# Performance work log

Hardware: AMD Instinct MI355X
Metric: run time of the kernel (lower is better)

Reference implementation:

```python
import jax, jax.numpy as jnp
import numpy as np

EPS = 1e-5

def layer_norm(x, gamma, beta):
    mu = jnp.mean(x, axis=-1, keepdims=True)
    var = jnp.mean(jnp.square(x - mu), axis=-1, keepdims=True)
    return (x - mu) * jax.lax.rsqrt(var + EPS) * gamma + beta

def reverse_sigmoid(x):
    # torch version clamps value to [0.001, 0.999] with a detached offset ->
    # straight-through: clipped value, identity gradient into the logit.
    y = x + jax.lax.stop_gradient(jnp.clip(x, 0.001, 0.999) - x)
    return jnp.log(y) - jnp.log1p(-y)

def setup_inputs() -> dict:
    key = jax.random.key(0)
    ks = jax.random.split(key, 8)
    N, D, A, F8, FD = 32768, 1024, 256, 8, 64
    inp = {
        "unary_term": jax.random.normal(ks[0], (N, D), jnp.float32),
        "pair_term": jax.random.normal(ks[1], (N, D), jnp.float32),
        "auxiliary_term": jax.random.normal(ks[2], (N, A), jnp.float32),
        "auxiliary_gating_weight": jax.random.uniform(ks[3], (N,), jnp.float32),
        # self.w params: LayerNorm(2D) + Linear(2D, FD)
        "ln_gamma": jnp.ones((2 * D,), jnp.float32),
        "ln_beta": jnp.zeros((2 * D,), jnp.float32),
        "W": jax.random.normal(ks[4], (2 * D, FD), jnp.float32) * 0.02,
        "b": jnp.zeros((FD,), jnp.float32),
        # self.w_aux params: LayerNorm(A) + Linear(A, 8)
        "ln_aux_gamma": jnp.ones((A,), jnp.float32),
        "ln_aux_beta": jnp.zeros((A,), jnp.float32),
        "W_aux": jax.random.normal(ks[5], (A, F8), jnp.float32) * 0.02,
        "b_aux": jnp.zeros((F8,), jnp.float32),
        # use_auxiliary_gate_weight=True -> both init to 0.33
        "gate_weight": jnp.array(0.33, jnp.float32),
        "aux_gate_weight": jnp.array(0.33, jnp.float32),
    }
    return inp

def reference(unary_term, pair_term, auxiliary_term, auxiliary_gating_weight,
              ln_gamma, ln_beta, W, b, ln_aux_gamma, ln_aux_beta, W_aux, b_aux,
              gate_weight, aux_gate_weight):
    # paired_feats = relu(cat([unary, pair], 1))
    paired = jax.nn.relu(jnp.concatenate([unary_term, pair_term], axis=1))  # [N, 2D]
    # gate = sigmoid(Linear(relu(LN(paired))))
    gate = jax.nn.sigmoid(jax.nn.relu(layer_norm(paired, ln_gamma, ln_beta)) @ W + b)  # [N, FD]
    aux_gate = jax.nn.sigmoid(jax.nn.relu(layer_norm(auxiliary_term, ln_aux_gamma, ln_aux_beta)) @ W_aux + b_aux)  # [N, 8]
    gate = jnp.mean(gate, axis=1)        # [N]
    aux_gate = jnp.mean(aux_gate, axis=1)  # [N]
    logit = gate_weight * reverse_sigmoid(gate) + aux_gate_weight * reverse_sigmoid(aux_gate)
    g = jax.nn.sigmoid(logit) * auxiliary_gating_weight  # use_auxiliary_gate_weight=True
    output = pair_term * g[:, None]
    return (output, g)
```

## Files before the change

kernel.cpp:

```cpp
#include <hip/hip_runtime.h>
#include <math.h>


#define EPS_LN 1e-5f

typedef __attribute__((ext_vector_type(8))) short short8;
typedef __attribute__((ext_vector_type(4))) float f32x4;

__device__ __forceinline__ unsigned short f2bf(float f) {
  unsigned int u = __float_as_uint(f);
  u += 0x7FFFu + ((u >> 16) & 1u);
  return (unsigned short)(u >> 16);
}

__device__ __forceinline__ float wsum64(float v) {
  v += __shfl_xor(v, 32);
  v += __shfl_xor(v, 16);
  v += __shfl_xor(v, 8);
  v += __shfl_xor(v, 4);
  v += __shfl_xor(v, 2);
  v += __shfl_xor(v, 1);
  return v;
}

__device__ __forceinline__ float sigmoidf_(float x) {
  return 1.0f / (1.0f + __expf(-x));
}

__device__ __forceinline__ float rsigf(float x) {
  float y = fminf(fmaxf(x, 0.001f), 0.999f);
  return logf(y) - log1pf(-y);
}

__device__ __forceinline__ short nrm1(float x, float g, float b,
                                      float rs, float nmr) {
  float t = fmaxf(x, 0.f);
  float n = fmaf(t, rs, nmr);
  float z = fmaxf(fmaf(n, g, b), 0.f);
  return (short)f2bf(z);
}

__global__ void prep_wfrag(const float* __restrict__ W,
                           unsigned short* __restrict__ wfrag) {
  const int lane = threadIdx.x;
  const int b = blockIdx.x;
  const int ntile = b >> 6;
  const int kb = b & 63;
  const int f = (ntile << 4) + (lane & 15);
  const int kbase = (kb << 5) + ((lane >> 4) << 3);
  unsigned short tmp[8];
#pragma unroll
  for (int j = 0; j < 8; ++j) tmp[j] = f2bf(W[(size_t)(kbase + j) * 64 + f]);
  ushort4* dst = reinterpret_cast<ushort4*>(wfrag + (((size_t)b * 64 + lane) << 3));
  dst[0] = make_ushort4(tmp[0], tmp[1], tmp[2], tmp[3]);
  dst[1] = make_ushort4(tmp[4], tmp[5], tmp[6], tmp[7]);
}

__global__ void __launch_bounds__(256, 4) fused_main(
    const float* __restrict__ unary, const float* __restrict__ pair,
    const float* __restrict__ aux, const float* __restrict__ auxw,
    const float* __restrict__ ln_g, const float* __restrict__ ln_b,
    const float* __restrict__ b_lin,
    const float* __restrict__ ln_ag, const float* __restrict__ ln_ab,
    const float* __restrict__ W_aux, const float* __restrict__ b_aux,
    const float* __restrict__ gw, const float* __restrict__ agw,
    const unsigned short* __restrict__ wfrag,
    float* __restrict__ out, float* __restrict__ out_g) {
  __shared__ float part[4][16][68];
  __shared__ float stat_mu[16];
  __shared__ float stat_rs[16];

  const int tid = threadIdx.x;
  const int w = tid >> 6;
  const int lane = tid & 63;
  const int base = blockIdx.x << 4;

  float auxg0 = 0.f, auxg1 = 0.f, auxg2 = 0.f, auxg3 = 0.f;

  const float4 agv4 = reinterpret_cast<const float4*>(ln_ag)[lane];
  const float4 abv4 = reinterpret_cast<const float4*>(ln_ab)[lane];
  const float bauxl = b_aux[lane & 7];

#pragma unroll
  for (int i = 0; i < 4; ++i) {
    const int rl = (w << 2) + i;
    const int row = base + rl;

    const float4* u4 = reinterpret_cast<const float4*>(unary + (size_t)row * 1024);
    const float4* p4 = reinterpret_cast<const float4*>(pair + (size_t)row * 1024);
    float s = 0.f, sq = 0.f;
#pragma unroll
    for (int j = 0; j < 4; ++j) {
      float4 uv = u4[lane + 64 * j];
      float4 pv = p4[lane + 64 * j];
      uv.x = fmaxf(uv.x, 0.f); uv.y = fmaxf(uv.y, 0.f);
      uv.z = fmaxf(uv.z, 0.f); uv.w = fmaxf(uv.w, 0.f);
      pv.x = fmaxf(pv.x, 0.f); pv.y = fmaxf(pv.y, 0.f);
      pv.z = fmaxf(pv.z, 0.f); pv.w = fmaxf(pv.w, 0.f);
      s += uv.x + uv.y + uv.z + uv.w;
      s += pv.x + pv.y + pv.z + pv.w;
      sq += uv.x * uv.x + uv.y * uv.y + uv.z * uv.z + uv.w * uv.w;
      sq += pv.x * pv.x + pv.y * pv.y + pv.z * pv.z + pv.w * pv.w;
    }
    s = wsum64(s);
    sq = wsum64(sq);
    const float mu = s * (1.f / 2048.f);
    const float rstd = rsqrtf(sq * (1.f / 2048.f) - mu * mu + EPS_LN);
    if (lane == 0) { stat_mu[rl] = mu; stat_rs[rl] = rstd; }

    const float4 av = reinterpret_cast<const float4*>(aux + (size_t)row * 256)[lane];
    float as = av.x + av.y + av.z + av.w;
    float asq = av.x * av.x + av.y * av.y + av.z * av.z + av.w * av.w;
    as = wsum64(as);
    asq = wsum64(asq);
    const float amu = as * (1.f / 256.f);
    const float arstd = rsqrtf(asq * (1.f / 256.f) - amu * amu + EPS_LN);
    float aa[4];
    aa[0] = fmaxf((av.x - amu) * arstd * agv4.x + abv4.x, 0.f);
    aa[1] = fmaxf((av.y - amu) * arstd * agv4.y + abv4.y, 0.f);
    aa[2] = fmaxf((av.z - amu) * arstd * agv4.z + abv4.z, 0.f);
    aa[3] = fmaxf((av.w - amu) * arstd * agv4.w + abv4.w, 0.f);
    float pf[8];
#pragma unroll
    for (int f = 0; f < 8; ++f) pf[f] = 0.f;
#pragma unroll
    for (int t = 0; t < 4; ++t) {
      const float4* wr = reinterpret_cast<const float4*>(W_aux + (((size_t)lane << 2) + t) * 8);
      float4 wa = wr[0], wb = wr[1];
      pf[0] += aa[t] * wa.x; pf[1] += aa[t] * wa.y;
      pf[2] += aa[t] * wa.z; pf[3] += aa[t] * wa.w;
      pf[4] += aa[t] * wb.x; pf[5] += aa[t] * wb.y;
      pf[6] += aa[t] * wb.z; pf[7] += aa[t] * wb.w;
    }
#pragma unroll
    for (int f = 0; f < 8; ++f) {
      pf[f] += __shfl_xor(pf[f], 1);
      pf[f] += __shfl_xor(pf[f], 2);
      pf[f] += __shfl_xor(pf[f], 4);
    }
    float v01 = (lane & 1) ? pf[1] : pf[0];
    float v23 = (lane & 1) ? pf[3] : pf[2];
    float v45 = (lane & 1) ? pf[5] : pf[4];
    float v67 = (lane & 1) ? pf[7] : pf[6];
    float v03 = (lane & 2) ? v23 : v01;
    float v47 = (lane & 2) ? v67 : v45;
    float v = (lane & 4) ? v47 : v03;
    v += __shfl_xor(v, 8);
    v += __shfl_xor(v, 16);
    v += __shfl_xor(v, 32);
    float sg = sigmoidf_(v + bauxl);
    sg += __shfl_xor(sg, 1);
    sg += __shfl_xor(sg, 2);
    sg += __shfl_xor(sg, 4);
    const float agv = sg * 0.125f;
    if (i == 0) auxg0 = agv;
    else if (i == 1) auxg1 = agv;
    else if (i == 2) auxg2 = agv;
    else auxg3 = agv;
  }

  __syncthreads();

  const int m = lane & 15;
  const int q = lane >> 4;
  const float mu = stat_mu[m];
  const float rs = stat_rs[m];
  const float nmr = -mu * rs;

  const float* srcp = (w < 2) ? unary : pair;
  const float* rowp = srcp + (size_t)(base + m) * 1024 + ((w & 1) << 9) + (q << 3);
  const float* gp = ln_g + (w << 9) + (q << 3);
  const float* bp = ln_b + (w << 9) + (q << 3);
  const unsigned short* wfp = wfrag + ((size_t)((w << 4) * 64 + lane) << 3);

  f32x4 acc[4] = {{0.f,0.f,0.f,0.f},{0.f,0.f,0.f,0.f},
                  {0.f,0.f,0.f,0.f},{0.f,0.f,0.f,0.f}};
#pragma unroll
  for (int kb = 0; kb < 16; ++kb) {
    const float4 x0 = *reinterpret_cast<const float4*>(rowp + (kb << 5));
    const float4 x1 = *reinterpret_cast<const float4*>(rowp + (kb << 5) + 4);
    const float4 g0 = *reinterpret_cast<const float4*>(gp + (kb << 5));
    const float4 g1 = *reinterpret_cast<const float4*>(gp + (kb << 5) + 4);
    const float4 b0 = *reinterpret_cast<const float4*>(bp + (kb << 5));
    const float4 b1 = *reinterpret_cast<const float4*>(bp + (kb << 5) + 4);
    short8 af;
    af[0] = nrm1(x0.x, g0.x, b0.x, rs, nmr);
    af[1] = nrm1(x0.y, g0.y, b0.y, rs, nmr);
    af[2] = nrm1(x0.z, g0.z, b0.z, rs, nmr);
    af[3] = nrm1(x0.w, g0.w, b0.w, rs, nmr);
    af[4] = nrm1(x1.x, g1.x, b1.x, rs, nmr);
    af[5] = nrm1(x1.y, g1.y, b1.y, rs, nmr);
    af[6] = nrm1(x1.z, g1.z, b1.z, rs, nmr);
    af[7] = nrm1(x1.w, g1.w, b1.w, rs, nmr);
#pragma unroll
    for (int nt = 0; nt < 4; ++nt) {
      const short8 bf = *reinterpret_cast<const short8*>(
          wfp + (size_t)nt * 32768 + (kb << 9));
      acc[nt] = __builtin_amdgcn_mfma_f32_16x16x32_bf16(af, bf, acc[nt], 0, 0, 0);
    }
  }

#pragma unroll
  for (int nt = 0; nt < 4; ++nt)
#pragma unroll
    for (int r = 0; r < 4; ++r)
      part[w][(q << 2) + r][(nt << 4) + m] = acc[nt][r];

  __syncthreads();

  const int rl = (w << 2) + q;
  const int f0 = m << 2;
  const float4 p0 = *reinterpret_cast<const float4*>(&part[0][rl][f0]);
  const float4 p1 = *reinterpret_cast<const float4*>(&part[1][rl][f0]);
  const float4 p2 = *reinterpret_cast<const float4*>(&part[2][rl][f0]);
  const float4 p3 = *reinterpret_cast<const float4*>(&part[3][rl][f0]);
  const float4 blv = reinterpret_cast<const float4*>(b_lin)[m];
  float sgs = sigmoidf_(p0.x + p1.x + p2.x + p3.x + blv.x)
            + sigmoidf_(p0.y + p1.y + p2.y + p3.y + blv.y)
            + sigmoidf_(p0.z + p1.z + p2.z + p3.z + blv.z)
            + sigmoidf_(p0.w + p1.w + p2.w + p3.w + blv.w);
  sgs += __shfl_xor(sgs, 1);
  sgs += __shfl_xor(sgs, 2);
  sgs += __shfl_xor(sgs, 4);
  sgs += __shfl_xor(sgs, 8);
  const float gate = sgs * (1.f / 64.f);
  const float auxg_r = (q == 0) ? auxg0 : (q == 1) ? auxg1
                     : (q == 2) ? auxg2 : auxg3;
  const float logit = gw[0] * rsigf(gate) + agw[0] * rsigf(auxg_r);
  const float g = sigmoidf_(logit) * auxw[base + rl];
  if (m == 0) out_g[base + rl] = g;

#pragma unroll
  for (int i = 0; i < 4; ++i) {
    const float gi = __shfl(g, i << 4);
    const int row = base + (w << 2) + i;
    const float4* pp = reinterpret_cast<const float4*>(pair + (size_t)row * 1024);
    float4* oo = reinterpret_cast<float4*>(out + (size_t)row * 1024);
#pragma unroll
    for (int j = 0; j < 4; ++j) {
      float4 pv = pp[lane + (j << 6)];
      pv.x *= gi; pv.y *= gi; pv.z *= gi; pv.w *= gi;
      oo[lane + (j << 6)] = pv;
    }
  }
}

extern "C" void kernel_launch(void* const* d_in, const int* in_sizes, int n_in,
                              void* d_out, int out_size, void* d_ws, size_t ws_size,
                              hipStream_t stream) {
  const float* unary = (const float*)d_in[0];
  const float* pair  = (const float*)d_in[1];
  const float* aux   = (const float*)d_in[2];
  const float* auxw  = (const float*)d_in[3];
  const float* ln_g  = (const float*)d_in[4];
  const float* ln_b  = (const float*)d_in[5];
  const float* W     = (const float*)d_in[6];
  const float* b     = (const float*)d_in[7];
  const float* ln_ag = (const float*)d_in[8];
  const float* ln_ab = (const float*)d_in[9];
  const float* W_aux = (const float*)d_in[10];
  const float* b_aux = (const float*)d_in[11];
  const float* gw    = (const float*)d_in[12];
  const float* agw   = (const float*)d_in[13];

  const int N = in_sizes[3];
  unsigned short* wfrag = (unsigned short*)d_ws;
  float* out = (float*)d_out;
  float* out_g = out + (size_t)N * 1024;

  prep_wfrag<<<256, 64, 0, stream>>>(W, wfrag);
  fused_main<<<N / 16, 256, 0, stream>>>(unary, pair, aux, auxw, ln_g, ln_b, b,
                                         ln_ag, ln_ab, W_aux, b_aux, gw, agw,
                                         wfrag, out, out_g);
}
```

Measured before the change: 435.8 us.

## Compute LayerNorm statistics and aux projection with MFMA instead of shuffles

LayerNorm sums and sums of squares for the main and auxiliary rows are now computed by MFMA against a ones matrix on bf16-packed inputs. The loads use the same per-lane fragment layout as the main GEMM, which replaces the per-row wave-shuffle reduction loop. The auxiliary Linear(256,8) now runs on MFMA using a bf16 fragment of W_aux prepared in the prep kernel, replacing scalar FMAs and shuffles. The statistics pass is meant to share the layout and cached lines of the GEMM pass, but it computes variance from bf16-rounded values, which costs precision, and the row data is still read twice.

Measured after the change: 425.4 us. 2.4% less time.

```diff
diff --git a/kernel.cpp b/kernel.cpp
--- a/kernel.cpp
+++ b/kernel.cpp
@@ -13,14 +13,26 @@
   return (unsigned short)(u >> 16);
 }
 
-__device__ __forceinline__ float wsum64(float v) {
-  v += __shfl_xor(v, 32);
-  v += __shfl_xor(v, 16);
-  v += __shfl_xor(v, 8);
-  v += __shfl_xor(v, 4);
-  v += __shfl_xor(v, 2);
-  v += __shfl_xor(v, 1);
-  return v;
+__device__ __forceinline__ unsigned pkbf2(float a, float b) {
+  unsigned ua = __float_as_uint(a), ub = __float_as_uint(b);
+  ua += 0x7FFFu + ((ua >> 16) & 1u);
+  ub += 0x7FFFu + ((ub >> 16) & 1u);
+  return (ub & 0xFFFF0000u) | (ua >> 16);
+}
+
+union S8U { unsigned u[4]; short8 v; };
+
+__device__ __forceinline__ short8 pack8(float x0, float x1, float x2, float x3,
+                                        float x4, float x5, float x6, float x7) {
+  S8U r;
+  r.u[0] = pkbf2(x0, x1); r.u[1] = pkbf2(x2, x3);
+  r.u[2] = pkbf2(x4, x5); r.u[3] = pkbf2(x6, x7);
+  return r.v;
+}
+
+__device__ __forceinline__ short8 ones8() {
+  S8U r; r.u[0] = r.u[1] = r.u[2] = r.u[3] = 0x3F803F80u;
+  return r.v;
 }
 
 __device__ __forceinline__ float sigmoidf_(float x) {
@@ -40,20 +52,34 @@
   return (short)f2bf(z);
 }
 
-__global__ void prep_wfrag(const float* __restrict__ W,
+__global__ void prep_frags(const float* __restrict__ W,
+                           const float* __restrict__ W_aux,
                            unsigned short* __restrict__ wfrag) {
   const int lane = threadIdx.x;
   const int b = blockIdx.x;
-  const int ntile = b >> 6;
-  const int kb = b & 63;
-  const int f = (ntile << 4) + (lane & 15);
-  const int kbase = (kb << 5) + ((lane >> 4) << 3);
   unsigned short tmp[8];
-#pragma unroll
-  for (int j = 0; j < 8; ++j) tmp[j] = f2bf(W[(size_t)(kbase + j) * 64 + f]);
-  ushort4* dst = reinterpret_cast<ushort4*>(wfrag + (((size_t)b * 64 + lane) << 3));
-  dst[0] = make_ushort4(tmp[0], tmp[1], tmp[2], tmp[3]);
-  dst[1] = make_ushort4(tmp[4], tmp[5], tmp[6], tmp[7]);
+  if (b < 256) {
+    const int ntile = b >> 6;
+    const int kb = b & 63;
+    const int f = (ntile << 4) + (lane & 15);
+    const int kbase = (kb << 5) + ((lane >> 4) << 3);
+#pragma unroll
+    for (int j = 0; j < 8; ++j) tmp[j] = f2bf(W[(size_t)(kbase + j) * 64 + f]);
+    ushort4* dst = reinterpret_cast<ushort4*>(wfrag + (((size_t)b * 64 + lane) << 3));
+    dst[0] = make_ushort4(tmp[0], tmp[1], tmp[2], tmp[3]);
+    dst[1] = make_ushort4(tmp[4], tmp[5], tmp[6], tmp[7]);
+  } else {
+    const int kb = b - 256;
+    const int f = lane & 15;
+    const int kbase = (kb << 5) + ((lane >> 4) << 3);
+#pragma unroll
+    for (int j = 0; j < 8; ++j)
+      tmp[j] = (f < 8) ? f2bf(W_aux[(size_t)(kbase + j) * 8 + f]) : (unsigned short)0;
+    ushort4* dst = reinterpret_cast<ushort4*>(wfrag + 131072 +
+                                              (((size_t)kb * 64 + lane) << 3));
+    dst[0] = make_ushort4(tmp[0], tmp[1], tmp[2], tmp[3]);
+    dst[1] = make_ushort4(tmp[4], tmp[5], tmp[6], tmp[7]);
+  }
 }
 
 __global__ void __launch_bounds__(256, 4) fused_main(
@@ -62,113 +88,81 @@
     const float* __restrict__ ln_g, const float* __restrict__ ln_b,
     const float* __restrict__ b_lin,
     const float* __restrict__ ln_ag, const float* __restrict__ ln_ab,
-    const float* __restrict__ W_aux, const float* __restrict__ b_aux,
+    const float* __restrict__ b_aux,
     const float* __restrict__ gw, const float* __restrict__ agw,
     const unsigned short* __restrict__ wfrag,
     float* __restrict__ out, float* __restrict__ out_g) {
   __shared__ float part[4][16][68];
-  __shared__ float stat_mu[16];
-  __shared__ float stat_rs[16];
+  __shared__ float auxpart[4][16][8];
+  __shared__ float4 statp[4][16];
 
   const int tid = threadIdx.x;
   const int w = tid >> 6;
   const int lane = tid & 63;
   const int base = blockIdx.x << 4;
-
-  float auxg0 = 0.f, auxg1 = 0.f, auxg2 = 0.f, auxg3 = 0.f;
-
-  const float4 agv4 = reinterpret_cast<const float4*>(ln_ag)[lane];
-  const float4 abv4 = reinterpret_cast<const float4*>(ln_ab)[lane];
-  const float bauxl = b_aux[lane & 7];
-
-#pragma unroll
-  for (int i = 0; i < 4; ++i) {
-    const int rl = (w << 2) + i;
-    const int row = base + rl;
-
-    const float4* u4 = reinterpret_cast<const float4*>(unary + (size_t)row * 1024);
-    const float4* p4 = reinterpret_cast<const float4*>(pair + (size_t)row * 1024);
-    float s = 0.f, sq = 0.f;
-#pragma unroll
-    for (int j = 0; j < 4; ++j) {
-      float4 uv = u4[lane + 64 * j];
-      float4 pv = p4[lane + 64 * j];
-      uv.x = fmaxf(uv.x, 0.f); uv.y = fmaxf(uv.y, 0.f);
-      uv.z = fmaxf(uv.z, 0.f); uv.w = fmaxf(uv.w, 0.f);
-      pv.x = fmaxf(pv.x, 0.f); pv.y = fmaxf(pv.y, 0.f);
-      pv.z = fmaxf(pv.z, 0.f); pv.w = fmaxf(pv.w, 0.f);
-      s += uv.x + uv.y + uv.z + uv.w;
-      s += pv.x + pv.y + pv.z + pv.w;
-      sq += uv.x * uv.x + uv.y * uv.y + uv.z * uv.z + uv.w * uv.w;
-      sq += pv.x * pv.x + pv.y * pv.y + pv.z * pv.z + pv.w * pv.w;
-    }
-    s = wsum64(s);
-    sq = wsum64(sq);
-    const float mu = s * (1.f / 2048.f);
-    const float rstd = rsqrtf(sq * (1.f / 2048.f) - mu * mu + EPS_LN);
-    if (lane == 0) { stat_mu[rl] = mu; stat_rs[rl] = rstd; }
-
-    const float4 av = reinterpret_cast<const float4*>(aux + (size_t)row * 256)[lane];
-    float as = av.x + av.y + av.z + av.w;
-    float asq = av.x * av.x + av.y * av.y + av.z * av.z + av.w * av.w;
-    as = wsum64(as);
-    asq = wsum64(asq);
-    const float amu = as * (1.f / 256.f);
-    const float arstd = rsqrtf(asq * (1.f / 256.f) - amu * amu + EPS_LN);
-    float aa[4];
-    aa[0] = fmaxf((av.x - amu) * arstd * agv4.x + abv4.x, 0.f);
-    aa[1] = fmaxf((av.y - amu) * arstd * agv4.y + abv4.y, 0.f);
-    aa[2] = fmaxf((av.z - amu) * arstd * agv4.z + abv4.z, 0.f);
-    aa[3] = fmaxf((av.w - amu) * arstd * agv4.w + abv4.w, 0.f);
-    float pf[8];
-#pragma unroll
-    for (int f = 0; f < 8; ++f) pf[f] = 0.f;
-#pragma unroll
-    for (int t = 0; t < 4; ++t) {
-      const float4* wr = reinterpret_cast<const float4*>(W_aux + (((size_t)lane << 2) + t) * 8);
-      float4 wa = wr[0], wb = wr[1];
-      pf[0] += aa[t] * wa.x; pf[1] += aa[t] * wa.y;
-      pf[2] += aa[t] * wa.z; pf[3] += aa[t] * wa.w;
-      pf[4] += aa[t] * wb.x; pf[5] += aa[t] * wb.y;
-      pf[6] += aa[t] * wb.z; pf[7] += aa[t] * wb.w;
-    }
-#pragma unroll
-    for (int f = 0; f < 8; ++f) {
-      pf[f] += __shfl_xor(pf[f], 1);
-      pf[f] += __shfl_xor(pf[f], 2);
-      pf[f] += __shfl_xor(pf[f], 4);
-    }
-    float v01 = (lane & 1) ? pf[1] : pf[0];
-    float v23 = (lane & 1) ? pf[3] : pf[2];
-    float v45 = (lane & 1) ? pf[5] : pf[4];
-    float v67 = (lane & 1) ? pf[7] : pf[6];
-    float v03 = (lane & 2) ? v23 : v01;
-    float v47 = (lane & 2) ? v67 : v45;
-    float v = (lane & 4) ? v47 : v03;
-    v += __shfl_xor(v, 8);
-    v += __shfl_xor(v, 16);
-    v += __shfl_xor(v, 32);
-    float sg = sigmoidf_(v + bauxl);
-    sg += __shfl_xor(sg, 1);
-    sg += __shfl_xor(sg, 2);
-    sg += __shfl_xor(sg, 4);
-    const float agv = sg * 0.125f;
-    if (i == 0) auxg0 = agv;
-    else if (i == 1) auxg1 = agv;
-    else if (i == 2) auxg2 = agv;
-    else auxg3 = agv;
-  }
-
-  __syncthreads();
-
   const int m = lane & 15;
   const int q = lane >> 4;
-  const float mu = stat_mu[m];
-  const float rs = stat_rs[m];
+
+  const float* srcp = (w < 2) ? unary : pair;
+  const float* arow = srcp + (size_t)(base + m) * 1024 + ((w & 1) << 9) + (q << 3);
+  const float* axrow = aux + (size_t)(base + m) * 256 + (w << 6) + (q << 3);
+
+  const short8 onef = ones8();
+
+  f32x4 aS = {0.f,0.f,0.f,0.f}, aQ = {0.f,0.f,0.f,0.f};
+  f32x4 sS = {0.f,0.f,0.f,0.f}, sQ = {0.f,0.f,0.f,0.f};
+  float axv[16];
+
+#pragma unroll
+  for (int kb = 0; kb < 2; ++kb) {
+    const float4 x0 = *reinterpret_cast<const float4*>(axrow + (kb << 5));
+    const float4 x1 = *reinterpret_cast<const float4*>(axrow + (kb << 5) + 4);
+    axv[kb * 8 + 0] = x0.x; axv[kb * 8 + 1] = x0.y;
+    axv[kb * 8 + 2] = x0.z; axv[kb * 8 + 3] = x0.w;
+    axv[kb * 8 + 4] = x1.x; axv[kb * 8 + 5] = x1.y;
+    axv[kb * 8 + 6] = x1.z; axv[kb * 8 + 7] = x1.w;
+    const short8 a = pack8(x0.x, x0.y, x0.z, x0.w, x1.x, x1.y, x1.z, x1.w);
+    const short8 a2 = pack8(x0.x * x0.x, x0.y * x0.y, x0.z * x0.z, x0.w * x0.w,
+                            x1.x * x1.x, x1.y * x1.y, x1.z * x1.z, x1.w * x1.w);
+    sS = __builtin_amdgcn_mfma_f32_16x16x32_bf16(a, onef, sS, 0, 0, 0);
+    sQ = __builtin_amdgcn_mfma_f32_16x16x32_bf16(a2, onef, sQ, 0, 0, 0);
+  }
+
+#pragma unroll
+  for (int kb = 0; kb < 16; ++kb) {
+    const float4 x0 = *reinterpret_cast<const float4*>(arow + (kb << 5));
+    const float4 x1 = *reinterpret_cast<const float4*>(arow + (kb << 5) + 4);
+    const float r0 = fmaxf(x0.x, 0.f), r1 = fmaxf(x0.y, 0.f);
+    const float r2 = fmaxf(x0.z, 0.f), r3 = fmaxf(x0.w, 0.f);
+    const float r4 = fmaxf(x1.x, 0.f), r5 = fmaxf(x1.y, 0.f);
+    const float r6 = fmaxf(x1.z, 0.f), r7 = fmaxf(x1.w, 0.f);
+    const short8 a = pack8(r0, r1, r2, r3, r4, r5, r6, r7);
+    const short8 a2 = pack8(r0 * r0, r1 * r1, r2 * r2, r3 * r3,
+                            r4 * r4, r5 * r5, r6 * r6, r7 * r7);
+    aS = __builtin_amdgcn_mfma_f32_16x16x32_bf16(a, onef, aS, 0, 0, 0);
+    aQ = __builtin_amdgcn_mfma_f32_16x16x32_bf16(a2, onef, aQ, 0, 0, 0);
+  }
+
+  if ((lane & 15) == 0) {
+    statp[w][(q << 2) + 0] = make_float4(aS[0], aQ[0], sS[0], sQ[0]);
+    statp[w][(q << 2) + 1] = make_float4(aS[1], aQ[1], sS[1], sQ[1]);
+    statp[w][(q << 2) + 2] = make_float4(aS[2], aQ[2], sS[2], sQ[2]);
+    statp[w][(q << 2) + 3] = make_float4(aS[3], aQ[3], sS[3], sQ[3]);
+  }
+  __syncthreads();
+
+  const float4 s0 = statp[0][m], s1 = statp[1][m], s2 = statp[2][m], s3 = statp[3][m];
+  const float S  = s0.x + s1.x + s2.x + s3.x;
+  const float Q  = s0.y + s1.y + s2.y + s3.y;
+  const float Sa = s0.z + s1.z + s2.z + s3.z;
+  const float Qa = s0.w + s1.w + s2.w + s3.w;
+  const float mu = S * (1.f / 2048.f);
+  const float rs = rsqrtf(Q * (1.f / 2048.f) - mu * mu + EPS_LN);
   const float nmr = -mu * rs;
-
-  const float* srcp = (w < 2) ? unary : pair;
-  const float* rowp = srcp + (size_t)(base + m) * 1024 + ((w & 1) << 9) + (q << 3);
+  const float amu = Sa * (1.f / 256.f);
+  const float ars = rsqrtf(Qa * (1.f / 256.f) - amu * amu + EPS_LN);
+  const float anmr = -amu * ars;
+
   const float* gp = ln_g + (w << 9) + (q << 3);
   const float* bp = ln_b + (w << 9) + (q << 3);
   const unsigned short* wfp = wfrag + ((size_t)((w << 4) * 64 + lane) << 3);
@@ -177,8 +171,8 @@
                   {0.f,0.f,0.f,0.f},{0.f,0.f,0.f,0.f}};
 #pragma unroll
   for (int kb = 0; kb < 16; ++kb) {
-    const float4 x0 = *reinterpret_cast<const float4*>(rowp + (kb << 5));
-    const float4 x1 = *reinterpret_cast<const float4*>(rowp + (kb << 5) + 4);
+    const float4 x0 = *reinterpret_cast<const float4*>(arow + (kb << 5));
+    const float4 x1 = *reinterpret_cast<const float4*>(arow + (kb << 5) + 4);
     const float4 g0 = *reinterpret_cast<const float4*>(gp + (kb << 5));
     const float4 g1 = *reinterpret_cast<const float4*>(gp + (kb << 5) + 4);
     const float4 b0 = *reinterpret_cast<const float4*>(bp + (kb << 5));
@@ -200,12 +194,40 @@
     }
   }
 
+  const float* agp = ln_ag + (w << 6) + (q << 3);
+  const float* abp = ln_ab + (w << 6) + (q << 3);
+  const unsigned short* afp = wfrag + 131072;
+  f32x4 acca = {0.f,0.f,0.f,0.f};
+#pragma unroll
+  for (int kb = 0; kb < 2; ++kb) {
+    const float4 g0 = *reinterpret_cast<const float4*>(agp + (kb << 5));
+    const float4 g1 = *reinterpret_cast<const float4*>(agp + (kb << 5) + 4);
+    const float4 b0 = *reinterpret_cast<const float4*>(abp + (kb << 5));
+    const float4 b1 = *reinterpret_cast<const float4*>(abp + (kb << 5) + 4);
+    short8 af;
+    af[0] = (short)f2bf(fmaxf(fmaf(fmaf(axv[kb*8+0], ars, anmr), g0.x, b0.x), 0.f));
+    af[1] = (short)f2bf(fmaxf(fmaf(fmaf(axv[kb*8+1], ars, anmr), g0.y, b0.y), 0.f));
+    af[2] = (short)f2bf(fmaxf(fmaf(fmaf(axv[kb*8+2], ars, anmr), g0.z, b0.z), 0.f));
+    af[3] = (short)f2bf(fmaxf(fmaf(fmaf(axv[kb*8+3], ars, anmr), g0.w, b0.w), 0.f));
+    af[4] = (short)f2bf(fmaxf(fmaf(fmaf(axv[kb*8+4], ars, anmr), g1.x, b1.x), 0.f));
+    af[5] = (short)f2bf(fmaxf(fmaf(fmaf(axv[kb*8+5], ars, anmr), g1.y, b1.y), 0.f));
+    af[6] = (short)f2bf(fmaxf(fmaf(fmaf(axv[kb*8+6], ars, anmr), g1.z, b1.z), 0.f));
+    af[7] = (short)f2bf(fmaxf(fmaf(fmaf(axv[kb*8+7], ars, anmr), g1.w, b1.w), 0.f));
+    const short8 bf = *reinterpret_cast<const short8*>(
+        afp + ((size_t)(((w << 1) + kb) * 64 + lane) << 3));
+    acca = __builtin_amdgcn_mfma_f32_16x16x32_bf16(af, bf, acca, 0, 0, 0);
+  }
+
 #pragma unroll
   for (int nt = 0; nt < 4; ++nt)
 #pragma unroll
     for (int r = 0; r < 4; ++r)
       part[w][(q << 2) + r][(nt << 4) + m] = acc[nt][r];
-
+  if (m < 8) {
+#pragma unroll
+    for (int r = 0; r < 4; ++r)
+      auxpart[w][(q << 2) + r][m] = acca[r];
+  }
   __syncthreads();
 
   const int rl = (w << 2) + q;
@@ -224,15 +246,25 @@
   sgs += __shfl_xor(sgs, 4);
   sgs += __shfl_xor(sgs, 8);
   const float gate = sgs * (1.f / 64.f);
-  const float auxg_r = (q == 0) ? auxg0 : (q == 1) ? auxg1
-                     : (q == 2) ? auxg2 : auxg3;
-  const float logit = gw[0] * rsigf(gate) + agw[0] * rsigf(auxg_r);
+
+  const int fa = m & 7;
+  float av4 = auxpart[0][rl][fa] + auxpart[1][rl][fa] +
+              auxpart[2][rl][fa] + auxpart[3][rl][fa];
+  float axs = sigmoidf_(av4 + b_aux[fa]);
+  axs = (m < 8) ? axs : 0.f;
+  axs += __shfl_xor(axs, 1);
+  axs += __shfl_xor(axs, 2);
+  axs += __shfl_xor(axs, 4);
+  axs += __shfl_xor(axs, 8);
+  const float auxg = axs * 0.125f;
+
+  const float logit = gw[0] * rsigf(gate) + agw[0] * rsigf(auxg);
   const float g = sigmoidf_(logit) * auxw[base + rl];
   if (m == 0) out_g[base + rl] = g;
 
 #pragma unroll
   for (int i = 0; i < 4; ++i) {
-    const float gi = __shfl(g, i << 4);
+    const float gi = __shfl(g, (i << 4));
     const int row = base + (w << 2) + i;
     const float4* pp = reinterpret_cast<const float4*>(pair + (size_t)row * 1024);
     float4* oo = reinterpret_cast<float4*>(out + (size_t)row * 1024);
@@ -268,8 +300,8 @@
   float* out = (float*)d_out;
   float* out_g = out + (size_t)N * 1024;
 
-  prep_wfrag<<<256, 64, 0, stream>>>(W, wfrag);
+  prep_frags<<<264, 64, 0, stream>>>(W, W_aux, wfrag);
   fused_main<<<N / 16, 256, 0, stream>>>(unary, pair, aux, auxw, ln_g, ln_b, b,
-                                         ln_ag, ln_ab, W_aux, b_aux, gw, agw,
+                                         ln_ag, ln_ab, b_aux, gw, agw,
                                          wfrag, out, out_g);
 }
```
